# Optimization experiments

Hardware: AMD Instinct MI355X
Metric: run time of the kernel (lower is better)

The kernel has to match this reference:

```python
import jax, jax.numpy as jnp
import numpy as np

H, HK, HD, WIN = 16, 4, 128, 512  # query heads, kv heads, head_dim, window
NEG = -1e30


def setup_inputs() -> dict:
    key = jax.random.key(0)
    ks = jax.random.split(key, 5)
    B, T, D = 2, 4096, 2048
    s = 1.0 / np.sqrt(D)
    return {
        "x": jax.random.normal(ks[0], (B, T, D), dtype=jnp.float32),
        "Wq": jax.random.normal(ks[1], (D, H * HD), dtype=jnp.float32) * s,
        "Wk": jax.random.normal(ks[2], (D, HK * HD), dtype=jnp.float32) * s,
        "Wv": jax.random.normal(ks[3], (D, HK * HD), dtype=jnp.float32) * s,
        "Wo": jax.random.normal(ks[4], (H * HD, D), dtype=jnp.float32) * s,
    }


def _local_attn(x, Wq, Wk, Wv, Wo):
    B, T, D = x.shape
    nrep = H // HK
    nb = T // WIN
    scale = 1.0 / np.sqrt(HD)

    q = (x @ Wq).reshape(B, nb, WIN, HK, nrep, HD)
    k = (x @ Wk).reshape(B, nb, WIN, HK, HD)
    v = (x @ Wv).reshape(B, nb, WIN, HK, HD)

    # each query block attends to its own block + the previous block,
    k_prev = jnp.concatenate([jnp.zeros_like(k[:, :1]), k[:, :-1]], axis=1)
    v_prev = jnp.concatenate([jnp.zeros_like(v[:, :1]), v[:, :-1]], axis=1)
    kcat = jnp.concatenate([k_prev, k], axis=2)  # [B,nb,2W,HK,HD]
    vcat = jnp.concatenate([v_prev, v], axis=2)

    r = jnp.arange(WIN)[:, None]       # query offset in block
    c = jnp.arange(2 * WIN)[None, :]   # key offset in concat window
    allowed = jnp.where(c < WIN, c > r, (c - WIN) <= r)  # [W,2W]
    first_block = (jnp.arange(nb) == 0)[:, None, None]   # block 0 has no prev
    allowed = allowed[None, :, :] & ~(first_block & (c < WIN)[None])  # [nb,W,2W]

    scores = jnp.einsum('bnqhrd,bnkhd->bnhrqk', q, kcat) * scale
    scores = jnp.where(allowed[None, :, None, None], scores, NEG)
    attn = jax.nn.softmax(scores, axis=-1)
    out = jnp.einsum('bnhrqk,bnkhd->bnqhrd', attn, vcat)
    out = out.reshape(B, T, H * HD)
    return out @ Wo


def reference(x, Wq, Wk, Wv, Wo):
    return _local_attn(x, Wq, Wk, Wv, Wo)
```

## Files before the change

kernel.cpp:

```cpp
#include <hip/hip_runtime.h>
#include <stdint.h>


typedef unsigned short u16;
typedef __attribute__((ext_vector_type(8))) short frag8;
typedef __attribute__((ext_vector_type(4))) float f32x4;

#define TILE 128

__device__ __forceinline__ u16 f2bf(float f) {
  union { float f; unsigned u; } c; c.f = f;
  unsigned u = c.u;
  return (u16)((u + 0x7fffu + ((u >> 16) & 1u)) >> 16);
}

__device__ __forceinline__ float fexp2(float x) {
  float r;
  asm("v_exp_f32 %0, %1" : "=v"(r) : "v"(x));
  return r;
}

__device__ __forceinline__ void async16(const u16* g, u16* l) {
  __builtin_amdgcn_global_load_lds((const __attribute__((address_space(1))) void*)g,
                                   (__attribute__((address_space(3))) void*)l, 16, 0, 0);
}

__device__ __forceinline__ void xcd_map(int& bx, int& by) {
  const int gx = gridDim.x;
  const int cx = gx >> 3;
  int id = blockIdx.y * gx + blockIdx.x;
  int xcd = id & 7, local = id >> 3;
  bx = xcd * cx + (local % cx);
  by = local / cx;
}

template <typename OutT>
__global__ __launch_bounds__(512, 2) void k_gemm256(const u16* __restrict__ A, int lda,
                                                    const u16* __restrict__ Bt, int ldb,
                                                    OutT* __restrict__ C, int ldc, int K,
                                                    float oscale) {
  __shared__ alignas(16) u16 Ab[2][256 * 64];
  __shared__ alignas(16) u16 Bb[2][256 * 64];
  const int tid = threadIdx.x, lane = tid & 63, wave = tid >> 6;
  const int wm = wave >> 2, wn = wave & 3;
  const int quad = lane >> 4, l16 = lane & 15;

  int bx, by;
  xcd_map(bx, by);

  const int rsub = wave * 8 + (lane >> 3);
  const int csub = ((lane & 7) ^ (lane >> 3)) * 8;
  const u16* Ag = A + ((long)bx * 256 + rsub) * lda + csub;
  const u16* Bg = Bt + ((long)by * 256 + rsub) * ldb + csub;
  const long a64 = (long)64 * lda, b64 = (long)64 * ldb;

  const int rsw = (l16 & 7) << 3;

  f32x4 acc[8][4];
#pragma unroll
  for (int i = 0; i < 8; ++i)
#pragma unroll
    for (int j = 0; j < 4; ++j) acc[i][j] = (f32x4){0.f, 0.f, 0.f, 0.f};

  const int nt = K >> 6;

#pragma unroll
  for (int c = 0; c < 4; ++c) {
    async16(Ag + c * a64, &Ab[0][c * 4096 + wave * 512]);
    async16(Bg + c * b64, &Bb[0][c * 4096 + wave * 512]);
  }

  for (int t = 0; t < nt; ++t) {
    const int buf = t & 1, nb = buf ^ 1;
    const long koff = (long)(t + 1) << 6;
    frag8 af[4][2], bf[2][2];

    if (t + 1 < nt) {
#pragma unroll
      for (int c = 0; c < 4; ++c) {
        async16(Ag + c * a64 + koff, &Ab[nb][c * 4096 + wave * 512]);
        async16(Bg + c * b64 + koff, &Bb[nb][c * 4096 + wave * 512]);
      }
      asm volatile("s_waitcnt vmcnt(8)" ::: "memory");
    } else {
      asm volatile("s_waitcnt vmcnt(0)" ::: "memory");
    }
    __builtin_amdgcn_s_barrier();
    asm volatile("" ::: "memory");

#pragma unroll
    for (int i = 0; i < 4; ++i)
#pragma unroll
      for (int kk = 0; kk < 2; ++kk)
        af[i][kk] = *(const frag8*)(&Ab[buf][(wm * 128 + i * 16 + l16) * 64 +
                                             ((kk * 32 + quad * 8) ^ rsw)]);
#pragma unroll
    for (int j = 0; j < 2; ++j)
#pragma unroll
      for (int kk = 0; kk < 2; ++kk)
        bf[j][kk] = *(const frag8*)(&Bb[buf][(wn * 64 + j * 16 + l16) * 64 +
                                             ((kk * 32 + quad * 8) ^ rsw)]);
    __builtin_amdgcn_s_setprio(1);
#pragma unroll
    for (int kk = 0; kk < 2; ++kk)
#pragma unroll
      for (int i = 0; i < 4; ++i)
#pragma unroll
        for (int j = 0; j < 2; ++j)
          acc[i][j] = __builtin_amdgcn_mfma_f32_16x16x32_bf16(af[i][kk], bf[j][kk], acc[i][j], 0, 0, 0);
    __builtin_amdgcn_s_setprio(0);
    __builtin_amdgcn_s_barrier();

#pragma unroll
    for (int j = 0; j < 2; ++j)
#pragma unroll
      for (int kk = 0; kk < 2; ++kk)
        bf[j][kk] = *(const frag8*)(&Bb[buf][(wn * 64 + (j + 2) * 16 + l16) * 64 +
                                             ((kk * 32 + quad * 8) ^ rsw)]);
    __builtin_amdgcn_s_setprio(1);
#pragma unroll
    for (int kk = 0; kk < 2; ++kk)
#pragma unroll
      for (int i = 0; i < 4; ++i)
#pragma unroll
        for (int j = 0; j < 2; ++j)
          acc[i][j + 2] = __builtin_amdgcn_mfma_f32_16x16x32_bf16(af[i][kk], bf[j][kk], acc[i][j + 2], 0, 0, 0);
    __builtin_amdgcn_s_setprio(0);
    __builtin_amdgcn_s_barrier();

#pragma unroll
    for (int i = 0; i < 4; ++i)
#pragma unroll
      for (int kk = 0; kk < 2; ++kk)
        af[i][kk] = *(const frag8*)(&Ab[buf][(wm * 128 + (i + 4) * 16 + l16) * 64 +
                                             ((kk * 32 + quad * 8) ^ rsw)]);
#pragma unroll
    for (int j = 0; j < 2; ++j)
#pragma unroll
      for (int kk = 0; kk < 2; ++kk)
        bf[j][kk] = *(const frag8*)(&Bb[buf][(wn * 64 + j * 16 + l16) * 64 +
                                             ((kk * 32 + quad * 8) ^ rsw)]);
    __builtin_amdgcn_s_setprio(1);
#pragma unroll
    for (int kk = 0; kk < 2; ++kk)
#pragma unroll
      for (int i = 0; i < 4; ++i)
#pragma unroll
        for (int j = 0; j < 2; ++j)
          acc[i + 4][j] = __builtin_amdgcn_mfma_f32_16x16x32_bf16(af[i][kk], bf[j][kk], acc[i + 4][j], 0, 0, 0);
    __builtin_amdgcn_s_setprio(0);
    __builtin_amdgcn_s_barrier();

#pragma unroll
    for (int j = 0; j < 2; ++j)
#pragma unroll
      for (int kk = 0; kk < 2; ++kk)
        bf[j][kk] = *(const frag8*)(&Bb[buf][(wn * 64 + (j + 2) * 16 + l16) * 64 +
                                             ((kk * 32 + quad * 8) ^ rsw)]);
    __builtin_amdgcn_s_setprio(1);
#pragma unroll
    for (int kk = 0; kk < 2; ++kk)
#pragma unroll
      for (int i = 0; i < 4; ++i)
#pragma unroll
        for (int j = 0; j < 2; ++j)
          acc[i + 4][j + 2] = __builtin_amdgcn_mfma_f32_16x16x32_bf16(af[i][kk], bf[j][kk], acc[i + 4][j + 2], 0, 0, 0);
    __builtin_amdgcn_s_setprio(0);
    __builtin_amdgcn_s_barrier();
  }

  OutT* Ct = C + ((long)bx * 256 + wm * 128) * ldc + (long)by * 256 + wn * 64;
#pragma unroll
  for (int i = 0; i < 8; ++i)
#pragma unroll
    for (int j = 0; j < 4; ++j) {
      int r0 = i * 16 + quad * 4, cc = j * 16 + l16;
#pragma unroll
      for (int r = 0; r < 4; ++r) {
        float v = acc[i][j][r] * oscale;
        if constexpr (sizeof(OutT) == 2)
          Ct[(long)(r0 + r) * ldc + cc] = f2bf(v);
        else
          Ct[(long)(r0 + r) * ldc + cc] = v;
      }
    }
}

__device__ __forceinline__ void gemm_core(const u16* __restrict__ A, int lda,
                                          const u16* __restrict__ Bt, int ldb,
                                          int K, u16* As, u16* Bs, f32x4 acc[4][4]) {
  const int tid = threadIdx.x;
  const int lane = tid & 63, wave = tid >> 6;
  const int wr = wave >> 1, wc = wave & 1;
  const int quad = lane >> 4, l16 = lane & 15;
#pragma unroll
  for (int i = 0; i < 4; ++i)
#pragma unroll
    for (int j = 0; j < 4; ++j) acc[i][j] = (f32x4){0.f, 0.f, 0.f, 0.f};

  const int row0 = tid >> 2, offc = (tid & 3) * 8;
  const int nt = K >> 5;

#pragma unroll
  for (int r = 0; r < 2; ++r) {
    int row = r * 64 + row0;
    async16(A + (long)row * lda + offc, As + r * 2048 + wave * 512);
    async16(Bt + (long)row * ldb + offc, Bs + r * 2048 + wave * 512);
  }

  for (int t = 0; t < nt; ++t) {
    const int bo = (t & 1) * 4096, nbo = bo ^ 4096;
    if (t + 1 < nt) {
      const int k0 = (t + 1) * 32;
#pragma unroll
      for (int r = 0; r < 2; ++r) {
        int row = r * 64 + row0;
        async16(A + (long)row * lda + k0 + offc, As + nbo + r * 2048 + wave * 512);
        async16(Bt + (long)row * ldb + k0 + offc, Bs + nbo + r * 2048 + wave * 512);
      }
      asm volatile("s_waitcnt vmcnt(4)" ::: "memory");
    } else {
      asm volatile("s_waitcnt vmcnt(0)" ::: "memory");
    }
    __builtin_amdgcn_s_barrier();
    asm volatile("" ::: "memory");

    frag8 af[4], bf[4];
#pragma unroll
    for (int i = 0; i < 4; ++i)
      af[i] = *(const frag8*)(As + bo + (wr * 64 + i * 16 + l16) * 32 + quad * 8);
#pragma unroll
    for (int j = 0; j < 4; ++j)
      bf[j] = *(const frag8*)(Bs + bo + (wc * 64 + j * 16 + l16) * 32 + quad * 8);
#pragma unroll
    for (int i = 0; i < 4; ++i)
#pragma unroll
      for (int j = 0; j < 4; ++j)
        acc[i][j] = __builtin_amdgcn_mfma_f32_16x16x32_bf16(af[i], bf[j], acc[i][j], 0, 0, 0);
    asm volatile("" ::: "memory");
    __builtin_amdgcn_s_barrier();
  }
}

#define EPI_COORDS                                             \
  const int lane = threadIdx.x & 63, wave = threadIdx.x >> 6;  \
  const int wr = wave >> 1, wc = wave & 1;                     \
  const int quad = lane >> 4, l16 = lane & 15;

__global__ __launch_bounds__(256) void k_gemm_bf16(const u16* __restrict__ A, int lda,
                                                   const u16* __restrict__ Bt, int ldb,
                                                   u16* __restrict__ C, int ldc, int K) {
  __shared__ alignas(16) u16 smem[4 * TILE * 32];
  int bx, by; xcd_map(bx, by);
  f32x4 acc[4][4];
  gemm_core(A + (long)bx * TILE * lda, lda,
            Bt + (long)by * TILE * ldb, ldb, K, smem, smem + 2 * TILE * 32, acc);
  EPI_COORDS
  u16* Ct = C + (long)bx * TILE * ldc + (long)by * TILE;
#pragma unroll
  for (int i = 0; i < 4; ++i)
#pragma unroll
    for (int j = 0; j < 4; ++j) {
      int r0 = wr * 64 + i * 16 + quad * 4, cc = wc * 64 + j * 16 + l16;
#pragma unroll
      for (int r = 0; r < 4; ++r) Ct[(long)(r0 + r) * ldc + cc] = f2bf(acc[i][j][r]);
    }
}

__global__ __launch_bounds__(256) void k_gemm_bf16t(const u16* __restrict__ A, int lda,
                                                    const u16* __restrict__ Bt, int ldb,
                                                    u16* __restrict__ Ct, int ldct, int K) {
  __shared__ alignas(16) u16 smem[4 * TILE * 32];
  int bx, by; xcd_map(bx, by);
  f32x4 acc[4][4];
  gemm_core(A + (long)bx * TILE * lda, lda,
            Bt + (long)by * TILE * ldb, ldb, K, smem, smem + 2 * TILE * 32, acc);
  EPI_COORDS
  u16* Cb = Ct + (long)by * TILE * ldct + (long)bx * TILE;
#pragma unroll
  for (int i = 0; i < 4; ++i)
#pragma unroll
    for (int j = 0; j < 4; ++j) {
      int n = wc * 64 + j * 16 + l16, m0 = wr * 64 + i * 16 + quad * 4;
      ushort4 o;
      o.x = f2bf(acc[i][j][0]); o.y = f2bf(acc[i][j][1]);
      o.z = f2bf(acc[i][j][2]); o.w = f2bf(acc[i][j][3]);
      *(ushort4*)(Cb + (long)n * ldct + m0) = o;
    }
}

__global__ __launch_bounds__(256, 2) void k_attn(const u16* __restrict__ qb,
                                                 const u16* __restrict__ kb,
                                                 const u16* __restrict__ vT,
                                                 u16* __restrict__ O) {
  __shared__ alignas(16) u16 Ks[2][64 * 128];
  __shared__ alignas(16) u16 Vs[128 * 64];
  __shared__ alignas(16) u16 Ps[4 * 32 * 64];
  const int tid = threadIdx.x, lane = tid & 63, wave = tid >> 6;
  const int quad = lane >> 4, l16 = lane & 15;

  const int id = blockIdx.x + 4 * blockIdx.y + 32 * blockIdx.z;
  const int g = (id & 7) | ((id >> 7) << 3);
  const int w = (id >> 3) & 15;
  const int hk = g & 3, blk = (g >> 2) & 7, b = g >> 5;
  const int h = hk * 4 + (w & 3), qi = w >> 2;

  const long tok_q = (long)b * 4096 + blk * 512 + qi * 128;

  frag8 qf[2][4];
#pragma unroll
  for (int i = 0; i < 2; ++i)
#pragma unroll
    for (int kt = 0; kt < 4; ++kt)
      qf[i][kt] = *(const frag8*)(qb + (tok_q + wave * 32 + i * 16 + l16) * 2048 +
                                  h * 128 + kt * 32 + quad * 8);

  frag8 onef;
#pragma unroll
  for (int e = 0; e < 8; ++e) onef[e] = (short)0x3F80;

  f32x4 o_acc[2][8], l_acc[2];
  float m_r[2][4];
#pragma unroll
  for (int i = 0; i < 2; ++i) {
#pragma unroll
    for (int j = 0; j < 8; ++j) o_acc[i][j] = (f32x4){0.f, 0.f, 0.f, 0.f};
    l_acc[i] = (f32x4){0.f, 0.f, 0.f, 0.f};
#pragma unroll
    for (int r = 0; r < 4; ++r) m_r[i][r] = 0.f;
  }

  const int rsw = (l16 & 7) << 3;

  auto stageK = [&](int buf, int ci) {
    const long tk = (long)b * 4096 + (blk - 1) * 512 + ci * 64;
#pragma unroll
    for (int c = 0; c < 4; ++c) {
      const int idx = (wave * 4 + c) * 512 + lane * 8;
      int row = idx >> 7, col = idx & 127;
      async16(kb + (tk + row) * 512 + hk * 128 + (col ^ ((row & 7) << 3)),
              &Ks[buf][(wave * 4 + c) * 512]);
    }
  };
  auto stageV = [&](int ci) {
    const long tk = (long)b * 4096 + (blk - 1) * 512 + ci * 64;
#pragma unroll
    for (int c = 0; c < 4; ++c) {
      const int idx = (wave * 4 + c) * 512 + lane * 8;
      int row = idx >> 6, col = idx & 63;
      async16(vT + ((long)hk * 128 + row) * 8192 + tk + (col ^ ((row & 7) << 3)),
              &Vs[(wave * 4 + c) * 512]);
    }
  };

  const int c0 = blk ? 2 * qi : 8, c1 = 9 + 2 * qi;
  int cur = 0;
  stageK(0, c0);
  stageV(c0);
  asm volatile("s_waitcnt vmcnt(0)" ::: "memory");
  __builtin_amdgcn_s_barrier();
  asm volatile("" ::: "memory");

  for (int ci = c0; ci <= c1; ++ci) {
    if (ci > c0) stageV(ci);
    if (ci < c1) stageK(cur ^ 1, ci + 1);

    f32x4 s_acc[2][4];
#pragma unroll
    for (int i = 0; i < 2; ++i)
#pragma unroll
      for (int j = 0; j < 4; ++j) s_acc[i][j] = (f32x4){0.f, 0.f, 0.f, 0.f};
#pragma unroll
    for (int kt = 0; kt < 4; ++kt) {
      frag8 bfr[4];
#pragma unroll
      for (int j = 0; j < 4; ++j)
        bfr[j] = *(const frag8*)(&Ks[cur][(j * 16 + l16) * 128 + ((kt * 32 + quad * 8) ^ rsw)]);
#pragma unroll
      for (int i = 0; i < 2; ++i)
#pragma unroll
        for (int j = 0; j < 4; ++j)
          s_acc[i][j] = __builtin_amdgcn_mfma_f32_16x16x32_bf16(qf[i][kt], bfr[j], s_acc[i][j], 0, 0, 0);
    }

    const bool prev = (ci < 8);
    const int doff = (prev ? ci * 64 : (ci - 8) * 64) - qi * 128;
    float mc[2][4];
#pragma unroll
    for (int i = 0; i < 2; ++i)
#pragma unroll
      for (int r = 0; r < 4; ++r) mc[i][r] = -1e30f;
    if (doff >= 0 && doff <= 64) {
#pragma unroll
      for (int i = 0; i < 2; ++i)
#pragma unroll
        for (int j = 0; j < 4; ++j)
#pragma unroll
          for (int r = 0; r < 4; ++r) {
            int rl = wave * 32 + i * 16 + quad * 4 + r;
            int lk = j * 16 + l16;
            bool ok = prev ? (lk + doff > rl) : (lk + doff <= rl);
            float s = ok ? s_acc[i][j][r] : -1e30f;
            s_acc[i][j][r] = s;
            mc[i][r] = fmaxf(mc[i][r], s);
          }
    } else {
#pragma unroll
      for (int i = 0; i < 2; ++i)
#pragma unroll
        for (int j = 0; j < 4; ++j)
#pragma unroll
          for (int r = 0; r < 4; ++r) mc[i][r] = fmaxf(mc[i][r], s_acc[i][j][r]);
    }

    bool need = false;
#pragma unroll
    for (int i = 0; i < 2; ++i)
#pragma unroll
      for (int r = 0; r < 4; ++r) need = need || (mc[i][r] > m_r[i][r] + 8.f);
    if (__any(need)) {
#pragma unroll
      for (int o = 1; o < 16; o <<= 1)
#pragma unroll
        for (int i = 0; i < 2; ++i)
#pragma unroll
          for (int r = 0; r < 4; ++r)
            mc[i][r] = fmaxf(mc[i][r], __shfl_xor(mc[i][r], o));
      float alpha[2][4];
#pragma unroll
      for (int i = 0; i < 2; ++i)
#pragma unroll
        for (int r = 0; r < 4; ++r) {
          float mn = fmaxf(m_r[i][r], mc[i][r]);
          alpha[i][r] = fexp2(m_r[i][r] - mn);
          m_r[i][r] = mn;
        }
#pragma unroll
      for (int i = 0; i < 2; ++i) {
#pragma unroll
        for (int j = 0; j < 8; ++j)
#pragma unroll
          for (int r = 0; r < 4; ++r) o_acc[i][j][r] *= alpha[i][r];
#pragma unroll
        for (int r = 0; r < 4; ++r) l_acc[i][r] *= alpha[i][r];
      }
    }

#pragma unroll
    for (int i = 0; i < 2; ++i)
#pragma unroll
      for (int j = 0; j < 4; ++j)
#pragma unroll
        for (int r = 0; r < 4; ++r)
          s_acc[i][j][r] = fexp2(s_acc[i][j][r] - m_r[i][r]);

    u16* PsW = &Ps[wave * 2048];
#pragma unroll
    for (int i = 0; i < 2; ++i)
#pragma unroll
      for (int r = 0; r < 4; ++r) {
        int xw = ((quad * 4 + r) & 7) << 3;
#pragma unroll
        for (int j = 0; j < 4; ++j)
          PsW[(i * 16 + quad * 4 + r) * 64 + ((j * 16 + l16) ^ xw)] = f2bf(s_acc[i][j][r]);
      }

    if (ci < c1)
      asm volatile("s_waitcnt vmcnt(4)" ::: "memory");
    else
      asm volatile("s_waitcnt vmcnt(0)" ::: "memory");

#pragma unroll
    for (int kt = 0; kt < 2; ++kt) {
      frag8 pf[2], vf[8];
#pragma unroll
      for (int i = 0; i < 2; ++i)
        pf[i] = *(const frag8*)(PsW + (i * 16 + l16) * 64 + ((kt * 32 + quad * 8) ^ rsw));
#pragma unroll
      for (int j = 0; j < 8; ++j)
        vf[j] = *(const frag8*)(&Vs[(j * 16 + l16) * 64 + ((kt * 32 + quad * 8) ^ rsw)]);
#pragma unroll
      for (int i = 0; i < 2; ++i) {
#pragma unroll
        for (int j = 0; j < 8; ++j)
          o_acc[i][j] = __builtin_amdgcn_mfma_f32_16x16x32_bf16(pf[i], vf[j], o_acc[i][j], 0, 0, 0);
        l_acc[i] = __builtin_amdgcn_mfma_f32_16x16x32_bf16(pf[i], onef, l_acc[i], 0, 0, 0);
      }
    }

    asm volatile("s_waitcnt vmcnt(0)" ::: "memory");
    __builtin_amdgcn_s_barrier();
    asm volatile("" ::: "memory");
    cur ^= 1;
  }

  float inv[2][4];
#pragma unroll
  for (int i = 0; i < 2; ++i)
#pragma unroll
    for (int r = 0; r < 4; ++r) inv[i][r] = 1.0f / l_acc[i][r];
  u16* Ob = &Ks[0][0];
#pragma unroll
  for (int i = 0; i < 2; ++i)
#pragma unroll
    for (int j = 0; j < 8; ++j)
#pragma unroll
      for (int r = 0; r < 4; ++r)
        Ob[(wave * 32 + i * 16 + quad * 4 + r) * 128 + j * 16 + l16] =
            f2bf(o_acc[i][j][r] * inv[i][r]);
  __syncthreads();
#pragma unroll
  for (int p = 0; p < 8; ++p) {
    int idx = p * 256 + tid;
    int row = idx >> 4, col = (idx & 15) * 8;
    *(frag8*)(O + (tok_q + row) * 2048 + h * 128 + col) = *(const frag8*)(Ob + row * 128 + col);
  }
}

__global__ void k_convert(const float4* __restrict__ x, ushort4* __restrict__ xb) {
  int i = blockIdx.x * 256 + threadIdx.x;
  float4 f = x[i];
  ushort4 o;
  o.x = f2bf(f.x); o.y = f2bf(f.y); o.z = f2bf(f.z); o.w = f2bf(f.w);
  xb[i] = o;
}

__global__ void k_transpose(const float* __restrict__ W, u16* __restrict__ WT, int K, int N) {
  __shared__ float sh[32][33];
  int n0 = blockIdx.x * 32, k0 = blockIdx.y * 32;
  int tx = threadIdx.x, ty = threadIdx.y;
#pragma unroll
  for (int i = 0; i < 32; i += 8) sh[ty + i][tx] = W[(long)(k0 + ty + i) * N + n0 + tx];
  __syncthreads();
#pragma unroll
  for (int i = 0; i < 32; i += 8) WT[(long)(n0 + ty + i) * K + k0 + tx] = f2bf(sh[tx][ty + i]);
}

extern "C" void kernel_launch(void* const* d_in, const int* in_sizes, int n_in,
                              void* d_out, int out_size, void* d_ws, size_t ws_size,
                              hipStream_t stream) {
  const float* x  = (const float*)d_in[0];
  const float* Wq = (const float*)d_in[1];
  const float* Wk = (const float*)d_in[2];
  const float* Wv = (const float*)d_in[3];
  const float* Wo = (const float*)d_in[4];
  float* out = (float*)d_out;

  const long BT = 8192, D = 2048, NKV = 512;
  size_t off = 0;
  auto alloc = [&](size_t bytes) -> char* {
    off = (off + 255) & ~(size_t)255;
    char* p = (char*)d_ws + off;
    off += bytes;
    return p;
  };

  u16* xb  = (u16*)alloc((size_t)BT * D * 2);
  u16* WqT = (u16*)alloc((size_t)D * D * 2);
  u16* WkT = (u16*)alloc((size_t)NKV * D * 2);
  u16* WvT = (u16*)alloc((size_t)NKV * D * 2);
  u16* WoT = (u16*)alloc((size_t)D * D * 2);
  u16* qb  = (u16*)alloc((size_t)BT * D * 2);
  u16* kb  = (u16*)alloc((size_t)BT * NKV * 2);
  u16* vT  = (u16*)alloc((size_t)NKV * BT * 2);
  u16* Oa  = xb;

  k_convert<<<16384, 256, 0, stream>>>((const float4*)x, (ushort4*)xb);
  dim3 tb(32, 8);
  k_transpose<<<dim3(64, 64), tb, 0, stream>>>(Wq, WqT, 2048, 2048);
  k_transpose<<<dim3(16, 64), tb, 0, stream>>>(Wk, WkT, 2048, 512);
  k_transpose<<<dim3(16, 64), tb, 0, stream>>>(Wv, WvT, 2048, 512);
  k_transpose<<<dim3(64, 64), tb, 0, stream>>>(Wo, WoT, 2048, 2048);

  const float qscale = 0.08838834764831845f * 1.4426950408889634f;
  k_gemm256<u16><<<dim3(32, 8), 512, 0, stream>>>(xb, 2048, WqT, 2048, qb, 2048, 2048,
                                                  qscale);
  k_gemm_bf16 <<<dim3(64, 4),  256, 0, stream>>>(xb, 2048, WkT, 2048, kb, 512, 2048);
  k_gemm_bf16t<<<dim3(64, 4),  256, 0, stream>>>(xb, 2048, WvT, 2048, vT, 8192, 2048);

  k_attn<<<dim3(4, 8, 32), 256, 0, stream>>>(qb, kb, vT, Oa);

  k_gemm256<float><<<dim3(32, 8), 512, 0, stream>>>(Oa, 2048, WoT, 2048, out, 2048, 2048,
                                                    1.0f);
}
```

Measured before the change: 422.0 us.

## Deepen k_gemm256 prefetch to two tiles and reuse fragments across quadrants

The 256x256 GEMM kernel now preloads two K tiles before the loop and issues each refill two iterations ahead, into the buffer just consumed. The A refill goes out after the last A reads and the B refill after the last B reads, so global loads spread across the MFMA phases. Quadrant order changes so the low and high A and B fragments are each read from LDS once per tile, where B fragments were read twice before. The cost is more registers for the extra fragments and tighter ordering between barriers and overwrites of a live buffer.

```diff
diff --git a/kernel.cpp b/kernel.cpp
--- a/kernel.cpp
+++ b/kernel.cpp
@@ -33,6 +33,8 @@
   bx = xcd * cx + (local % cx);
   by = local / cx;
 }
+
+#define FENCE asm volatile("" ::: "memory")
 
 template <typename OutT>
 __global__ __launch_bounds__(512, 2) void k_gemm256(const u16* __restrict__ A, int lda,
@@ -69,104 +71,121 @@
     async16(Ag + c * a64, &Ab[0][c * 4096 + wave * 512]);
     async16(Bg + c * b64, &Bb[0][c * 4096 + wave * 512]);
   }
+#pragma unroll
+  for (int c = 0; c < 4; ++c) {
+    async16(Ag + c * a64 + 64, &Ab[1][c * 4096 + wave * 512]);
+    async16(Bg + c * b64 + 64, &Bb[1][c * 4096 + wave * 512]);
+  }
+  asm volatile("s_waitcnt vmcnt(8)" ::: "memory");
+  __builtin_amdgcn_s_barrier();
+  FENCE;
 
   for (int t = 0; t < nt; ++t) {
-    const int buf = t & 1, nb = buf ^ 1;
-    const long koff = (long)(t + 1) << 6;
-    frag8 af[4][2], bf[2][2];
-
-    if (t + 1 < nt) {
-#pragma unroll
-      for (int c = 0; c < 4; ++c) {
-        async16(Ag + c * a64 + koff, &Ab[nb][c * 4096 + wave * 512]);
-        async16(Bg + c * b64 + koff, &Bb[nb][c * 4096 + wave * 512]);
-      }
+    const int buf = t & 1;
+    const bool st = (t + 2 < nt);
+    const long koff = (long)(t + 2) << 6;
+    frag8 af_lo[4][2], af_hi[4][2], bf_lo[2][2], bf_hi[2][2];
+
+#pragma unroll
+    for (int i = 0; i < 4; ++i)
+#pragma unroll
+      for (int kk = 0; kk < 2; ++kk)
+        af_lo[i][kk] = *(const frag8*)(&Ab[buf][(wm * 128 + i * 16 + l16) * 64 +
+                                               ((kk * 32 + quad * 8) ^ rsw)]);
+#pragma unroll
+    for (int j = 0; j < 2; ++j)
+#pragma unroll
+      for (int kk = 0; kk < 2; ++kk)
+        bf_lo[j][kk] = *(const frag8*)(&Bb[buf][(wn * 64 + j * 16 + l16) * 64 +
+                                               ((kk * 32 + quad * 8) ^ rsw)]);
+    FENCE;
+    __builtin_amdgcn_s_barrier();
+    FENCE;
+    __builtin_amdgcn_s_setprio(1);
+#pragma unroll
+    for (int kk = 0; kk < 2; ++kk)
+#pragma unroll
+      for (int i = 0; i < 4; ++i)
+#pragma unroll
+        for (int j = 0; j < 2; ++j)
+          acc[i][j] = __builtin_amdgcn_mfma_f32_16x16x32_bf16(af_lo[i][kk], bf_lo[j][kk], acc[i][j], 0, 0, 0);
+    __builtin_amdgcn_s_setprio(0);
+    FENCE;
+    __builtin_amdgcn_s_barrier();
+    FENCE;
+
+#pragma unroll
+    for (int i = 0; i < 4; ++i)
+#pragma unroll
+      for (int kk = 0; kk < 2; ++kk)
+        af_hi[i][kk] = *(const frag8*)(&Ab[buf][(wm * 128 + (i + 4) * 16 + l16) * 64 +
+                                               ((kk * 32 + quad * 8) ^ rsw)]);
+    FENCE;
+    __builtin_amdgcn_s_barrier();
+    FENCE;
+    __builtin_amdgcn_s_setprio(1);
+#pragma unroll
+    for (int kk = 0; kk < 2; ++kk)
+#pragma unroll
+      for (int i = 0; i < 4; ++i)
+#pragma unroll
+        for (int j = 0; j < 2; ++j)
+          acc[i + 4][j] = __builtin_amdgcn_mfma_f32_16x16x32_bf16(af_hi[i][kk], bf_lo[j][kk], acc[i + 4][j], 0, 0, 0);
+    __builtin_amdgcn_s_setprio(0);
+    FENCE;
+    __builtin_amdgcn_s_barrier();
+    FENCE;
+
+#pragma unroll
+    for (int j = 0; j < 2; ++j)
+#pragma unroll
+      for (int kk = 0; kk < 2; ++kk)
+        bf_hi[j][kk] = *(const frag8*)(&Bb[buf][(wn * 64 + (j + 2) * 16 + l16) * 64 +
+                                               ((kk * 32 + quad * 8) ^ rsw)]);
+    if (st) {
+#pragma unroll
+      for (int c = 0; c < 4; ++c)
+        async16(Ag + c * a64 + koff, &Ab[buf][c * 4096 + wave * 512]);
+    }
+    FENCE;
+    __builtin_amdgcn_s_barrier();
+    FENCE;
+    __builtin_amdgcn_s_setprio(1);
+#pragma unroll
+    for (int kk = 0; kk < 2; ++kk)
+#pragma unroll
+      for (int i = 0; i < 4; ++i)
+#pragma unroll
+        for (int j = 0; j < 2; ++j)
+          acc[i][j + 2] = __builtin_amdgcn_mfma_f32_16x16x32_bf16(af_lo[i][kk], bf_hi[j][kk], acc[i][j + 2], 0, 0, 0);
+    __builtin_amdgcn_s_setprio(0);
+    FENCE;
+    __builtin_amdgcn_s_barrier();
+    FENCE;
+
+    if (st) {
+#pragma unroll
+      for (int c = 0; c < 4; ++c)
+        async16(Bg + c * b64 + koff, &Bb[buf][c * 4096 + wave * 512]);
+    }
+    FENCE;
+    __builtin_amdgcn_s_barrier();
+    FENCE;
+    __builtin_amdgcn_s_setprio(1);
+#pragma unroll
+    for (int kk = 0; kk < 2; ++kk)
+#pragma unroll
+      for (int i = 0; i < 4; ++i)
+#pragma unroll
+        for (int j = 0; j < 2; ++j)
+          acc[i + 4][j + 2] = __builtin_amdgcn_mfma_f32_16x16x32_bf16(af_hi[i][kk], bf_hi[j][kk], acc[i + 4][j + 2], 0, 0, 0);
+    __builtin_amdgcn_s_setprio(0);
+    if (st)
       asm volatile("s_waitcnt vmcnt(8)" ::: "memory");
-    } else {
+    else
       asm volatile("s_waitcnt vmcnt(0)" ::: "memory");
-    }
-    __builtin_amdgcn_s_barrier();
-    asm volatile("" ::: "memory");
-
-#pragma unroll
-    for (int i = 0; i < 4; ++i)
-#pragma unroll
-      for (int kk = 0; kk < 2; ++kk)
-        af[i][kk] = *(const frag8*)(&Ab[buf][(wm * 128 + i * 16 + l16) * 64 +
-                                             ((kk * 32 + quad * 8) ^ rsw)]);
-#pragma unroll
-    for (int j = 0; j < 2; ++j)
-#pragma unroll
-      for (int kk = 0; kk < 2; ++kk)
-        bf[j][kk] = *(const frag8*)(&Bb[buf][(wn * 64 + j * 16 + l16) * 64 +
-                                             ((kk * 32 + quad * 8) ^ rsw)]);
-    __builtin_amdgcn_s_setprio(1);
-#pragma unroll
-    for (int kk = 0; kk < 2; ++kk)
-#pragma unroll
-      for (int i = 0; i < 4; ++i)
-#pragma unroll
-        for (int j = 0; j < 2; ++j)
-          acc[i][j] = __builtin_amdgcn_mfma_f32_16x16x32_bf16(af[i][kk], bf[j][kk], acc[i][j], 0, 0, 0);
-    __builtin_amdgcn_s_setprio(0);
-    __builtin_amdgcn_s_barrier();
-
-#pragma unroll
-    for (int j = 0; j < 2; ++j)
-#pragma unroll
-      for (int kk = 0; kk < 2; ++kk)
-        bf[j][kk] = *(const frag8*)(&Bb[buf][(wn * 64 + (j + 2) * 16 + l16) * 64 +
-                                             ((kk * 32 + quad * 8) ^ rsw)]);
-    __builtin_amdgcn_s_setprio(1);
-#pragma unroll
-    for (int kk = 0; kk < 2; ++kk)
-#pragma unroll
-      for (int i = 0; i < 4; ++i)
-#pragma unroll
-        for (int j = 0; j < 2; ++j)
-          acc[i][j + 2] = __builtin_amdgcn_mfma_f32_16x16x32_bf16(af[i][kk], bf[j][kk], acc[i][j + 2], 0, 0, 0);
-    __builtin_amdgcn_s_setprio(0);
-    __builtin_amdgcn_s_barrier();
-
-#pragma unroll
-    for (int i = 0; i < 4; ++i)
-#pragma unroll
-      for (int kk = 0; kk < 2; ++kk)
-        af[i][kk] = *(const frag8*)(&Ab[buf][(wm * 128 + (i + 4) * 16 + l16) * 64 +
-                                             ((kk * 32 + quad * 8) ^ rsw)]);
-#pragma unroll
-    for (int j = 0; j < 2; ++j)
-#pragma unroll
-      for (int kk = 0; kk < 2; ++kk)
-        bf[j][kk] = *(const frag8*)(&Bb[buf][(wn * 64 + j * 16 + l16) * 64 +
-                                             ((kk * 32 + quad * 8) ^ rsw)]);
-    __builtin_amdgcn_s_setprio(1);
-#pragma unroll
-    for (int kk = 0; kk < 2; ++kk)
-#pragma unroll
-      for (int i = 0; i < 4; ++i)
-#pragma unroll
-        for (int j = 0; j < 2; ++j)
-          acc[i + 4][j] = __builtin_amdgcn_mfma_f32_16x16x32_bf16(af[i][kk], bf[j][kk], acc[i + 4][j], 0, 0, 0);
-    __builtin_amdgcn_s_setprio(0);
-    __builtin_amdgcn_s_barrier();
-
-#pragma unroll
-    for (int j = 0; j < 2; ++j)
-#pragma unroll
-      for (int kk = 0; kk < 2; ++kk)
-        bf[j][kk] = *(const frag8*)(&Bb[buf][(wn * 64 + (j + 2) * 16 + l16) * 64 +
-                                             ((kk * 32 + quad * 8) ^ rsw)]);
-    __builtin_amdgcn_s_setprio(1);
-#pragma unroll
-    for (int kk = 0; kk < 2; ++kk)
-#pragma unroll
-      for (int i = 0; i < 4; ++i)
-#pragma unroll
-        for (int j = 0; j < 2; ++j)
-          acc[i + 4][j + 2] = __builtin_amdgcn_mfma_f32_16x16x32_bf16(af[i][kk], bf[j][kk], acc[i + 4][j + 2], 0, 0, 0);
-    __builtin_amdgcn_s_setprio(0);
-    __builtin_amdgcn_s_barrier();
+    __builtin_amdgcn_s_barrier();
+    FENCE;
   }
 
   OutT* Ct = C + ((long)bx * 256 + wm * 128) * ldc + (long)by * 256 + wn * 64;
@@ -223,7 +242,7 @@
       asm volatile("s_waitcnt vmcnt(0)" ::: "memory");
     }
     __builtin_amdgcn_s_barrier();
-    asm volatile("" ::: "memory");
+    FENCE;
 
     frag8 af[4], bf[4];
 #pragma unroll
@@ -237,7 +256,7 @@
 #pragma unroll
       for (int j = 0; j < 4; ++j)
         acc[i][j] = __builtin_amdgcn_mfma_f32_16x16x32_bf16(af[i], bf[j], acc[i][j], 0, 0, 0);
-    asm volatile("" ::: "memory");
+    FENCE;
     __builtin_amdgcn_s_barrier();
   }
 }
@@ -359,7 +378,7 @@
   stageV(c0);
   asm volatile("s_waitcnt vmcnt(0)" ::: "memory");
   __builtin_amdgcn_s_barrier();
-  asm volatile("" ::: "memory");
+  FENCE;
 
   for (int ci = c0; ci <= c1; ++ci) {
     if (ci > c0) stageV(ci);
@@ -490,7 +509,7 @@
 
     asm volatile("s_waitcnt vmcnt(0)" ::: "memory");
     __builtin_amdgcn_s_barrier();
-    asm volatile("" ::: "memory");
+    FENCE;
     cur ^= 1;
   }
 
```

After: 404.9 us. -4.1%, faster.
